# Kernel optimization log

Hardware: AMD Instinct MI355X
Metric: run time of the kernel (lower is better)

Reference implementation:

```python
import jax, jax.numpy as jnp
import numpy as np

K_MIN = 30.0
TAU = 1e-06
BETA = 0.9
LAMBDA_MAX = 0.1
LAMBDA_SCALE = 1.0

N, D_OUT, N_MODULES, N_CONTEXTS = 262144, 128, 64, 16


def setup_inputs() -> dict:
    key = jax.random.key(0)
    k1, k2, k3, k4 = jax.random.split(key, 4)
    Y_hat = jax.random.normal(k1, (N, D_OUT), dtype=jnp.float32)
    context_weights = jax.random.uniform(k2, (N, N_CONTEXTS), dtype=jnp.float32)
    M_pinv = jax.random.normal(k3, (N_MODULES, D_OUT), dtype=jnp.float32) * 0.1
    C_prior = jax.random.normal(k4, (N_CONTEXTS, N_MODULES, N_MODULES), dtype=jnp.float32) * 0.1
    # Buffers exactly as registered in __init__
    ema_Sigma = jnp.broadcast_to(jnp.eye(N_MODULES, dtype=jnp.float32), (N_CONTEXTS, N_MODULES, N_MODULES))
    ema_sigma_sq = jnp.ones((N_CONTEXTS, N_MODULES), dtype=jnp.float32)
    ema_initialized = jnp.zeros((N_CONTEXTS,), dtype=bool)
    return {"Y_hat": Y_hat, "context_weights": context_weights, "M_pinv": M_pinv,
            "C_prior": C_prior, "ema_Sigma": ema_Sigma, "ema_sigma_sq": ema_sigma_sq,
            "ema_initialized": ema_initialized}


def reference(Y_hat, context_weights, M_pinv, C_prior, ema_Sigma, ema_sigma_sq, ema_initialized):
    # Z_hat: [N, m]
    Z = Y_hat @ M_pinv.T
    wsum = context_weights.sum(axis=0)            # [T] == eff_n per context
    active = wsum >= K_MIN                        # context skipping, vectorized
    # Weighted mean per context: [T, m]
    mu = (context_weights.T @ Z) / wsum[:, None]
    # Weighted covariance: sum_n w_norm * (z-mu)(z-mu)^T == E_w[zz^T] - mu mu^T
    w_norm = context_weights / wsum[None, :]      # [N, T]
    S = jnp.einsum('nt,nm,nk->tmk', w_norm, Z, Z)  # [T, m, m]
    Sigma = S - mu[:, :, None] * mu[:, None, :]
    # EMA sigma_sq update (no-grad in original -> stop_gradient)
    Sigma_sg = jax.lax.stop_gradient(Sigma)
    diag_init = jnp.diagonal(Sigma_sg, axis1=1, axis2=2)                       # first-call branch
    diag_ema = jnp.diagonal(BETA * ema_Sigma + (1.0 - BETA) * Sigma_sg, axis1=1, axis2=2)
    sigma_sq = jnp.where(ema_initialized[:, None], diag_ema, diag_init)        # [T, m]
    std = jnp.sqrt(sigma_sq + TAU)
    denom = std[:, :, None] * std[:, None, :]
    C_hat = jnp.clip(Sigma / (denom + TAU), -1.0, 1.0)
    loss_t = jnp.sum((C_hat - C_prior) ** 2, axis=(1, 2)) / wsum               # [T]
    n_active = jnp.sum(active)
    total = jnp.sum(jnp.where(active, loss_t, 0.0))
    total = jnp.where(n_active > 0,
                      LAMBDA_MAX * LAMBDA_SCALE * total / jnp.maximum(n_active, 1).astype(total.dtype),
                      jnp.zeros((), total.dtype))
    return total
```

## Files before the change

### kernel.cpp

```cpp
#include <hip/hip_runtime.h>
#include <stdint.h>

#define N_ROWS 262144
#define D_OUTC 128
#define M_MOD  64
#define T_CTX  16

#define ZB_OFF   ((size_t)0)
#define ZB_BYTES ((size_t)M_MOD * N_ROWS * 2)
#define WT_OFF   (ZB_OFF + ZB_BYTES)
#define WT_BYTES ((size_t)T_CTX * N_ROWS * 2)
#define SS_OFF   (WT_OFF + WT_BYTES)
#define SS_BYTES ((size_t)T_CTX * M_MOD * M_MOD * 4)
#define B_OFF    (SS_OFF + SS_BYTES)
#define B_BYTES  ((size_t)T_CTX * M_MOD * 4)
#define WSUM_OFF (B_OFF + B_BYTES)
#define WSUM_BYTES ((size_t)64)
#define LT_OFF   (WSUM_OFF + WSUM_BYTES)
#define LT_BYTES ((size_t)64)
#define PSS_OFF  (LT_OFF + LT_BYTES)
#define PSS_BYTES ((size_t)256 * T_CTX * M_MOD * M_MOD * 2)
#define NEED_BIG (PSS_OFF + PSS_BYTES)

typedef __attribute__((ext_vector_type(4))) float f32x4;
typedef __attribute__((ext_vector_type(8))) _Float16 f16x8;
typedef __attribute__((ext_vector_type(2))) _Float16 h2;

union FR { uint4 u; f16x8 v; h2 h[4]; };

__device__ __forceinline__ float bf2f(unsigned short u) {
  return __uint_as_float(((unsigned int)u) << 16);
}
__device__ __forceinline__ unsigned short f2bf(float f) {
  unsigned int x = __float_as_uint(f);
  return (unsigned short)((x + 0x7fffu + ((x >> 16) & 1u)) >> 16);
}
__device__ __forceinline__ h2 cvt_pkrtz(float a, float b) {
  return __builtin_bit_cast(h2, __builtin_amdgcn_cvt_pkrtz(a, b));
}
#if __has_builtin(__builtin_amdgcn_fdot2)
__device__ __forceinline__ float fdot2f(h2 a, h2 b, float c) {
  return __builtin_amdgcn_fdot2(a, b, c, false);
}
#else
__device__ __forceinline__ float fdot2f(h2 a, h2 b, float c) {
  return c + (float)a[0] * (float)b[0] + (float)a[1] * (float)b[1];
}
#endif

#define WAITVM(N) asm volatile("s_waitcnt vmcnt(" #N ")" ::: "memory")
#define SBAR() do { __builtin_amdgcn_s_barrier(); __builtin_amdgcn_sched_barrier(0); } while (0)

__global__ __launch_bounds__(256, 3) void zk_kernel(
    const float* __restrict__ Y, const float* __restrict__ Mp,
    const float* __restrict__ W,
    _Float16* __restrict__ Zbt, _Float16* __restrict__ Wt,
    float* __restrict__ Bm0 )
{
  __shared__ __align__(16) float    Yl[64 * 128];
  __shared__ __align__(16) _Float16 Mpl[64 * 128];
  __shared__ float Wf[16][65];
  const int tid  = threadIdx.x;
  const int l    = tid & 63;
  const int wv   = tid >> 6;
  const int g    = l >> 4;
  const int col  = l & 15;
  const int n0   = blockIdx.x * 64;

  if (blockIdx.x == 0) {
    float4 z4 = {0.f, 0.f, 0.f, 0.f};
    float4* p = (float4*)Bm0;
    p[tid] = z4;
    if (tid < 4) p[256 + tid] = z4;
  }

#pragma unroll
  for (int k = 0; k < 8; ++k) {
    const int pr  = wv * 8 + k;
    const int row = pr * 2 + (l >> 5);
    const int q   = l & 31;
    const int b   = (q & ~7) | ((q & 7) ^ (row & 7));
    const float* src = Y + ((size_t)(n0 + row)) * D_OUTC + b * 4;
    __builtin_amdgcn_global_load_lds((const unsigned int*)src,
        (unsigned int*)((char*)&Yl[0] + pr * 1024), 16, 0, 0);
  }
  {
    const int m  = tid >> 2;
    const int dq = tid & 3;
#pragma unroll
    for (int i = 0; i < 4; ++i) {
      const int s = dq * 4 + i;
      const float* mp = Mp + (size_t)m * D_OUTC + s * 8;
      float4 a = *(const float4*)mp;
      float4 b = *(const float4*)(mp + 4);
      FR o;
      o.h[0] = cvt_pkrtz(a.x, a.y); o.h[1] = cvt_pkrtz(a.z, a.w);
      o.h[2] = cvt_pkrtz(b.x, b.y); o.h[3] = cvt_pkrtz(b.z, b.w);
      const int ss = (s & ~7) | ((s & 7) ^ (m & 7));
      *(uint4*)((char*)&Mpl[0] + m * 256 + ss * 16) = o.u;
    }
  }
  {
    const int r  = tid >> 2;
    const int c0 = (tid & 3) * 4;
    float4 wv4 = *(const float4*)(W + (size_t)(n0 + r) * T_CTX + c0);
    Wf[c0 + 0][r] = wv4.x; Wf[c0 + 1][r] = wv4.y;
    Wf[c0 + 2][r] = wv4.z; Wf[c0 + 3][r] = wv4.w;
  }
  __syncthreads();
  {
    const int t = tid >> 4, ni = tid & 15;
    h2 h0 = cvt_pkrtz(Wf[t][4 * ni], Wf[t][4 * ni + 1]);
    h2 h1 = cvt_pkrtz(Wf[t][4 * ni + 2], Wf[t][4 * ni + 3]);
    uint2 pk = {__builtin_bit_cast(unsigned int, h0), __builtin_bit_cast(unsigned int, h1)};
    *(uint2*)(Wt + (size_t)t * N_ROWS + n0 + 4 * ni) = pk;
  }
  f32x4 acc[4];
#pragma unroll
  for (int qi = 0; qi < 4; ++qi) acc[qi] = (f32x4){0.f, 0.f, 0.f, 0.f};
  const int nrow = wv * 16 + col;
#pragma unroll
  for (int ks = 0; ks < 4; ++ks) {
    const char* yb = (const char*)&Yl[0] + nrow * 512 + ks * 128;
    uint4 y0 = *(const uint4*)(yb + 16 * ((2 * g) ^ (nrow & 7)));
    uint4 y1 = *(const uint4*)(yb + 16 * ((2 * g + 1) ^ (nrow & 7)));
    const float* f0 = (const float*)&y0;
    const float* f1 = (const float*)&y1;
    FR B;
    B.h[0] = cvt_pkrtz(f0[0], f0[1]); B.h[1] = cvt_pkrtz(f0[2], f0[3]);
    B.h[2] = cvt_pkrtz(f1[0], f1[1]); B.h[3] = cvt_pkrtz(f1[2], f1[3]);
#pragma unroll
    for (int qi = 0; qi < 4; ++qi) {
      const int m = qi * 16 + col;
      const int s = ks * 4 + g;
      FR A;
      A.u = *(const uint4*)((char*)&Mpl[0] + m * 256 + 16 * ((s & ~7) | ((s & 7) ^ (m & 7))));
      acc[qi] = __builtin_amdgcn_mfma_f32_16x16x32_f16(A.v, B.v, acc[qi], 0, 0, 0);
    }
  }
#pragma unroll
  for (int qi = 0; qi < 4; ++qi)
#pragma unroll
    for (int i = 0; i < 4; ++i)
      Zbt[(size_t)(qi * 16 + g * 4 + i) * N_ROWS + n0 + wv * 16 + col] =
          (_Float16)acc[qi][i];
}

#define SS_NS 256
#define NCH   16
template <bool PARTIAL>
__global__ __launch_bounds__(512, 4) void ss_kernel(
    const _Float16* __restrict__ Zbt, const _Float16* __restrict__ Wt,
    float* __restrict__ SS, float* __restrict__ Bm,
    unsigned short* __restrict__ Pss)
{
  __shared__ __align__(16) _Float16 Zl[4][64 * 64];
  __shared__ __align__(16) _Float16 Wlds[8 * 1024];
  const int tid = threadIdx.x;
  const int l   = tid & 63;
  const int wv  = tid >> 6;
  const int g   = l >> 4;
  const int col = l & 15;
  const int ns  = blockIdx.x & (SS_NS - 1);
  const int cg  = blockIdx.x >> 8;
  const int ctx = cg * 8 + wv;
  const int n0b = ns * 1024;

  f32x4 acc[4][4];
  f32x4 accB[4];
#pragma unroll
  for (int a = 0; a < 4; ++a) {
    accB[a] = (f32x4){0.f, 0.f, 0.f, 0.f};
#pragma unroll
    for (int b = 0; b < 4; ++b) acc[a][b] = (f32x4){0.f, 0.f, 0.f, 0.f};
  }
  FR ones;
#pragma unroll
  for (int j = 0; j < 4; ++j) ones.h[j] = (h2){(_Float16)1.f, (_Float16)1.f};

#pragma unroll
  for (int k = 0; k < 2; ++k) {
    const _Float16* wsrc = Wt + (size_t)ctx * N_ROWS + n0b + k * 512 + l * 8;
    __builtin_amdgcn_global_load_lds((const unsigned int*)wsrc,
        (unsigned int*)((char*)Wlds + wv * 2048 + k * 1024), 16, 0, 0);
  }
  const int zrow  = 8 * wv + (l >> 3);
  const int zslot = l & 7;
  auto stage = [&](int c) {
    const int n0 = n0b + c * 64;
    const _Float16* src = Zbt + (size_t)zrow * N_ROWS + n0 + 8 * (zslot ^ (zrow & 7));
    __builtin_amdgcn_global_load_lds((const unsigned int*)src,
        (unsigned int*)((char*)&Zl[c & 3][0] + wv * 1024 + l * 16), 16, 0, 0);
  };

  stage(0); stage(1); stage(2);
  WAITVM(2);
  SBAR();

  for (int c = 0; c < NCH; ++c) {
    if (c + 3 < NCH) stage(c + 3);
    const char* zb = (const char*)&Zl[c & 3][0];
    const char* wb = (const char*)Wlds + wv * 2048 + c * 128;
#pragma unroll
    for (int s = 0; s < 2; ++s) {
      FR wfr;
      wfr.u = *(const uint4*)(wb + s * 64 + g * 16);
      FR fr[4];
#pragma unroll
      for (int qi = 0; qi < 4; ++qi) {
        const int r = qi * 16 + col;
        fr[qi].u = *(const uint4*)(zb + r * 128 + 16 * ((s * 4 + g) ^ (r & 7)));
      }
      __builtin_amdgcn_s_setprio(1);
#pragma unroll
      for (int qi = 0; qi < 4; ++qi) {
        FR A;
#pragma unroll
        for (int j = 0; j < 4; ++j) A.h[j] = fr[qi].h[j] * wfr.h[j];
        accB[qi] = __builtin_amdgcn_mfma_f32_16x16x32_f16(A.v, ones.v, accB[qi], 0, 0, 0);
#pragma unroll
        for (int ki = 0; ki < 4; ++ki)
          acc[qi][ki] = __builtin_amdgcn_mfma_f32_16x16x32_f16(A.v, fr[ki].v, acc[qi][ki], 0, 0, 0);
      }
      __builtin_amdgcn_s_setprio(0);
    }
    if (c + 3 < NCH)       { WAITVM(2); SBAR(); }
    else if (c == NCH - 3) { WAITVM(1); SBAR(); }
    else if (c == NCH - 2) { WAITVM(0); SBAR(); }
  }

  if (col == 0) {
#pragma unroll
    for (int qi = 0; qi < 4; ++qi)
#pragma unroll
      for (int i = 0; i < 4; ++i)
        atomicAdd(&Bm[ctx * 64 + qi * 16 + g * 4 + i], accB[qi][i]);
  }
  if (PARTIAL) {
    unsigned short* P = Pss + ((size_t)ns * 16 + ctx) * 4096;
#pragma unroll
    for (int qi = 0; qi < 4; ++qi)
#pragma unroll
      for (int ki = 0; ki < 4; ++ki)
#pragma unroll
        for (int i = 0; i < 4; ++i)
          P[(qi * 16 + g * 4 + i) * 64 + ki * 16 + col] = f2bf(acc[qi][ki][i]);
  } else {
#pragma unroll
    for (int qi = 0; qi < 4; ++qi)
#pragma unroll
      for (int ki = 0; ki < 4; ++ki)
#pragma unroll
        for (int i = 0; i < 4; ++i)
          atomicAdd(&SS[(size_t)ctx * 4096 + (qi * 16 + g * 4 + i) * 64 + ki * 16 + col],
                    acc[qi][ki][i]);
  }
}

__global__ __launch_bounds__(256) void ssredw_kernel(
    const unsigned short* __restrict__ Pss, float* __restrict__ SS,
    const _Float16* __restrict__ Wt, float* __restrict__ wsum)
{
  const int tid = threadIdx.x;
  if (blockIdx.x < 256) {
    const int e = blockIdx.x * 256 + tid;
    float s = 0.f;
#pragma unroll 8
    for (int b = 0; b < 256; ++b)
      s += bf2f(Pss[(size_t)b * 65536 + e]);
    SS[e] = s;
  } else {
    const int b2 = blockIdx.x - 256;
    const int t = b2 >> 2, q = b2 & 3;
    const uint4* base = (const uint4*)(Wt + (size_t)t * N_ROWS + q * 65536);
    const h2 one2 = {(_Float16)1.f, (_Float16)1.f};
    float s = 0.f;
    for (int i = tid; i < 8192; i += 256) {
      uint4 v = base[i];
      const h2* h = (const h2*)&v;
#pragma unroll
      for (int j = 0; j < 4; ++j) s = fdot2f(h[j], one2, s);
    }
    s += __shfl_xor(s, 1);  s += __shfl_xor(s, 2);
    s += __shfl_xor(s, 4);  s += __shfl_xor(s, 8);
    s += __shfl_xor(s, 16); s += __shfl_xor(s, 32);
    __shared__ float red[4];
    if ((tid & 63) == 0) red[tid >> 6] = s;
    __syncthreads();
    if (tid == 0) atomicAdd(&wsum[t], red[0] + red[1] + red[2] + red[3]);
  }
}

__global__ __launch_bounds__(256) void wsk_kernel(const _Float16* __restrict__ Wt,
                                                  float* __restrict__ wsum)
{
  const int tid = threadIdx.x;
  const int t = blockIdx.x >> 2, q = blockIdx.x & 3;
  const uint4* base = (const uint4*)(Wt + (size_t)t * N_ROWS + q * 65536);
  const h2 one2 = {(_Float16)1.f, (_Float16)1.f};
  float s = 0.f;
  for (int i = tid; i < 8192; i += 256) {
    uint4 v = base[i];
    const h2* h = (const h2*)&v;
#pragma unroll
    for (int j = 0; j < 4; ++j) s = fdot2f(h[j], one2, s);
  }
  s += __shfl_xor(s, 1);  s += __shfl_xor(s, 2);
  s += __shfl_xor(s, 4);  s += __shfl_xor(s, 8);
  s += __shfl_xor(s, 16); s += __shfl_xor(s, 32);
  __shared__ float red[4];
  if ((tid & 63) == 0) red[tid >> 6] = s;
  __syncthreads();
  if (tid == 0) atomicAdd(&wsum[t], red[0] + red[1] + red[2] + red[3]);
}

__global__ __launch_bounds__(64) void fin1_kernel(
    const float* __restrict__ SS, const float* __restrict__ Bm,
    const float* __restrict__ wsum, const float* __restrict__ Cp,
    const float* __restrict__ emaS, const unsigned char* __restrict__ inited,
    float* __restrict__ LT)
{
  const int t = blockIdx.x, m = threadIdx.x;
  __shared__ float muL[64], stdL[64];
  const float ws  = wsum[t];
  const float inv = 1.0f / ws;
  const float mu  = Bm[t * 64 + m] * inv;
  {
    float Smm = SS[(size_t)t * 4096 + m * 65] * inv - mu * mu;
    float de  = 0.9f * emaS[(size_t)t * 4096 + m * 65] + 0.1f * Smm;
    float sq  = inited[t] ? de : Smm;
    muL[m]  = mu;
    stdL[m] = sqrtf(sq + 1e-6f);
  }
  __syncthreads();
  const float sm = stdL[m];
  const float* SSr = SS + (size_t)t * 4096 + m * 64;
  const float* Cpr = Cp + (size_t)t * 4096 + m * 64;
  float acc = 0.f;
#pragma unroll
  for (int k = 0; k < 64; ++k) {
    float Sig = SSr[k] * inv - mu * muL[k];
    float den = sm * stdL[k] + 1e-6f;
    float ch  = fminf(1.f, fmaxf(-1.f, Sig / den));
    float d   = ch - Cpr[k];
    acc = fmaf(d, d, acc);
  }
#pragma unroll
  for (int o = 1; o < 64; o <<= 1) acc += __shfl_xor(acc, o);
  if (m == 0) LT[t] = acc * inv;
}

__global__ __launch_bounds__(64) void fin2_kernel(
    const float* __restrict__ LT, const float* __restrict__ wsum,
    float* __restrict__ out)
{
  const int l = threadIdx.x;
  float lt = 0.f, act = 0.f;
  if (l < 16) {
    float ws = wsum[l];
    if (ws >= 30.0f) { act = 1.f; lt = LT[l]; }
  }
#pragma unroll
  for (int o = 1; o < 16; o <<= 1) {
    lt  += __shfl_xor(lt, o);
    act += __shfl_xor(act, o);
  }
  if (l == 0) out[0] = (act > 0.f) ? (0.1f * 1.0f * lt / act) : 0.f;
}

extern "C" void kernel_launch(void* const* d_in, const int* in_sizes, int n_in,
                              void* d_out, int out_size, void* d_ws, size_t ws_size,
                              hipStream_t stream) {
  (void)in_sizes; (void)n_in; (void)out_size;
  const float* Y    = (const float*)d_in[0];
  const float* W    = (const float*)d_in[1];
  const float* Mp   = (const float*)d_in[2];
  const float* Cp   = (const float*)d_in[3];
  const float* emaS = (const float*)d_in[4];
  const unsigned char* inited = (const unsigned char*)d_in[6];
  float* out = (float*)d_out;
  char* ws = (char*)d_ws;
  _Float16* Zbt = (_Float16*)(ws + ZB_OFF);
  _Float16* Wt  = (_Float16*)(ws + WT_OFF);
  float* SS   = (float*)(ws + SS_OFF);
  float* Bm   = (float*)(ws + B_OFF);
  float* wsum = (float*)(ws + WSUM_OFF);
  float* LT   = (float*)(ws + LT_OFF);
  unsigned short* Pss = (unsigned short*)(ws + PSS_OFF);

  if (ws_size >= NEED_BIG) {
    zk_kernel<<<N_ROWS / 64, 256, 0, stream>>>(Y, Mp, W, Zbt, Wt, Bm);
    ss_kernel<true><<<2 * SS_NS, 512, 0, stream>>>(Zbt, Wt, SS, Bm, Pss);
    ssredw_kernel<<<320, 256, 0, stream>>>(Pss, SS, Wt, wsum);
  } else {
    (void)hipMemsetAsync(ws + SS_OFF, 0, SS_BYTES, stream);
    zk_kernel<<<N_ROWS / 64, 256, 0, stream>>>(Y, Mp, W, Zbt, Wt, Bm);
    ss_kernel<false><<<2 * SS_NS, 512, 0, stream>>>(Zbt, Wt, SS, Bm, Pss);
    wsk_kernel<<<64, 256, 0, stream>>>(Wt, wsum);
  }
  fin1_kernel<<<16, 64, 0, stream>>>(SS, Bm, wsum, Cp, emaS, inited, LT);
  fin2_kernel<<<1, 64, 0, stream>>>(LT, wsum, out);
}
```

Baseline: 126.7 us.

## Fuse finalization into reduction kernel via last-block ticket

Folds the two small finalize kernels into the partial-sum reduction kernel. The last block to finish, found with an atomic ticket counter, computes per-context covariance normalization, correlation clipping and loss, then writes the output. The counter sits in the zeroed workspace region, which is extended to cover it. This removes two kernel launches and their gaps, at the cost of a serial 16-context loop run in a single block plus threadfence overhead.

```diff
diff --git a/kernel.cpp b/kernel.cpp
--- a/kernel.cpp
+++ b/kernel.cpp
@@ -18,7 +18,9 @@
 #define WSUM_BYTES ((size_t)64)
 #define LT_OFF   (WSUM_OFF + WSUM_BYTES)
 #define LT_BYTES ((size_t)64)
-#define PSS_OFF  (LT_OFF + LT_BYTES)
+#define CNT_OFF  (LT_OFF + LT_BYTES)
+#define CNT_BYTES ((size_t)64)
+#define PSS_OFF  (CNT_OFF + CNT_BYTES)
 #define PSS_BYTES ((size_t)256 * T_CTX * M_MOD * M_MOD * 2)
 #define NEED_BIG (PSS_OFF + PSS_BYTES)
 
@@ -71,7 +73,7 @@
     float4 z4 = {0.f, 0.f, 0.f, 0.f};
     float4* p = (float4*)Bm0;
     p[tid] = z4;
-    if (tid < 4) p[256 + tid] = z4;
+    if (tid < 12) p[256 + tid] = z4;
   }
 
 #pragma unroll
@@ -257,9 +259,12 @@
   }
 }
 
-__global__ __launch_bounds__(256) void ssredw_kernel(
+__global__ __launch_bounds__(256) void ssredfin_kernel(
     const unsigned short* __restrict__ Pss, float* __restrict__ SS,
-    const _Float16* __restrict__ Wt, float* __restrict__ wsum)
+    const _Float16* __restrict__ Wt, float* __restrict__ wsum,
+    const float* __restrict__ Bm, const float* __restrict__ Cp,
+    const float* __restrict__ emaS, const unsigned char* __restrict__ inited,
+    float* __restrict__ out, unsigned int* __restrict__ cnt)
 {
   const int tid = threadIdx.x;
   if (blockIdx.x < 256) {
@@ -284,11 +289,62 @@
     s += __shfl_xor(s, 1);  s += __shfl_xor(s, 2);
     s += __shfl_xor(s, 4);  s += __shfl_xor(s, 8);
     s += __shfl_xor(s, 16); s += __shfl_xor(s, 32);
-    __shared__ float red[4];
-    if ((tid & 63) == 0) red[tid >> 6] = s;
+    __shared__ float redw[4];
+    if ((tid & 63) == 0) redw[tid >> 6] = s;
     __syncthreads();
-    if (tid == 0) atomicAdd(&wsum[t], red[0] + red[1] + red[2] + red[3]);
-  }
+    if (tid == 0) atomicAdd(&wsum[t], redw[0] + redw[1] + redw[2] + redw[3]);
+  }
+
+  __threadfence();
+  __shared__ unsigned int ticket;
+  if (tid == 0) ticket = atomicAdd(cnt, 1u);
+  __syncthreads();
+  if (ticket != 319u) return;
+  __threadfence();
+
+  __shared__ float wsl[16];
+  __shared__ float muL[64], stdL[64];
+  __shared__ float bred[4];
+  if (tid < 16) wsl[tid] = wsum[tid];
+  __syncthreads();
+  float out_acc = 0.f, act_cnt = 0.f;
+  for (int t = 0; t < 16; ++t) {
+    const float ws  = wsl[t];
+    const float inv = 1.0f / ws;
+    if (tid < 64) {
+      float mu  = Bm[t * 64 + tid] * inv;
+      float Smm = SS[(size_t)t * 4096 + tid * 65] * inv - mu * mu;
+      float de  = 0.9f * emaS[(size_t)t * 4096 + tid * 65] + 0.1f * Smm;
+      float sq  = inited[t] ? de : Smm;
+      muL[tid]  = mu;
+      stdL[tid] = sqrtf(sq + 1e-6f);
+    }
+    __syncthreads();
+    const int m  = tid >> 2;
+    const int k0 = (tid & 3) * 16;
+    const float* SSr = SS + (size_t)t * 4096 + m * 64;
+    const float* Cpr = Cp + (size_t)t * 4096 + m * 64;
+    float acc = 0.f;
+#pragma unroll
+    for (int j = 0; j < 16; ++j) {
+      const int k = k0 + j;
+      float Sig = SSr[k] * inv - muL[m] * muL[k];
+      float den = stdL[m] * stdL[k] + 1e-6f;
+      float ch  = fminf(1.f, fmaxf(-1.f, Sig / den));
+      float d   = ch - Cpr[k];
+      acc = fmaf(d, d, acc);
+    }
+#pragma unroll
+    for (int o = 1; o < 64; o <<= 1) acc += __shfl_xor(acc, o);
+    if ((tid & 63) == 0) bred[tid >> 6] = acc;
+    __syncthreads();
+    if (tid == 0) {
+      float lt = (bred[0] + bred[1] + bred[2] + bred[3]) * inv;
+      if (ws >= 30.0f) { out_acc += lt; act_cnt += 1.f; }
+    }
+    __syncthreads();
+  }
+  if (tid == 0) out[0] = (act_cnt > 0.f) ? (0.1f * out_acc / act_cnt) : 0.f;
 }
 
 __global__ __launch_bounds__(256) void wsk_kernel(const _Float16* __restrict__ Wt,
@@ -386,18 +442,20 @@
   float* Bm   = (float*)(ws + B_OFF);
   float* wsum = (float*)(ws + WSUM_OFF);
   float* LT   = (float*)(ws + LT_OFF);
+  unsigned int* cnt = (unsigned int*)(ws + CNT_OFF);
   unsigned short* Pss = (unsigned short*)(ws + PSS_OFF);
 
   if (ws_size >= NEED_BIG) {
     zk_kernel<<<N_ROWS / 64, 256, 0, stream>>>(Y, Mp, W, Zbt, Wt, Bm);
     ss_kernel<true><<<2 * SS_NS, 512, 0, stream>>>(Zbt, Wt, SS, Bm, Pss);
-    ssredw_kernel<<<320, 256, 0, stream>>>(Pss, SS, Wt, wsum);
+    ssredfin_kernel<<<320, 256, 0, stream>>>(Pss, SS, Wt, wsum, Bm, Cp, emaS,
+                                             inited, out, cnt);
   } else {
     (void)hipMemsetAsync(ws + SS_OFF, 0, SS_BYTES, stream);
     zk_kernel<<<N_ROWS / 64, 256, 0, stream>>>(Y, Mp, W, Zbt, Wt, Bm);
     ss_kernel<false><<<2 * SS_NS, 512, 0, stream>>>(Zbt, Wt, SS, Bm, Pss);
     wsk_kernel<<<64, 256, 0, stream>>>(Wt, wsum);
-  }
-  fin1_kernel<<<16, 64, 0, stream>>>(SS, Bm, wsum, Cp, emaS, inited, LT);
-  fin2_kernel<<<1, 64, 0, stream>>>(LT, wsum, out);
-}
+    fin1_kernel<<<16, 64, 0, stream>>>(SS, Bm, wsum, Cp, emaS, inited, LT);
+    fin2_kernel<<<1, 64, 0, stream>>>(LT, wsum, out);
+  }
+}
```

Result: slower. 179.4 us (+41.5%).
